# Kernel optimization log

Measured on AMD Instinct MI355X. Metric: run time of the kernel, lower is better.

The kernel has to match this reference:

```python
import jax, jax.numpy as jnp
import numpy as np

N = 20000      # nodes
E = 120000     # directed edges (self-loops added in reference, per PyG default)
F_IN = 235
HID = 256
HEADS = 8
NEG_SLOPE = 0.2


def setup_inputs() -> dict:
    key = jax.random.key(0)
    ks = jax.random.split(key, 24)
    p = lambda k, shape: (jax.random.normal(k, shape, jnp.float32) * 0.05)
    inp = {}
    inp["x"] = jax.random.normal(ks[0], (N, F_IN), jnp.float32)
    inp["edge_index"] = jax.random.randint(ks[1], (2, E), 0, N, jnp.int32)
    # input projection
    inp["w_in"] = p(ks[2], (F_IN, HID)); inp["b_in"] = jnp.zeros((HID,), jnp.float32)
    # temporal MLP
    inp["w_t1"] = p(ks[3], (HID, HID)); inp["b_t1"] = jnp.zeros((HID,), jnp.float32)
    inp["w_t2"] = p(ks[4], (HID, HID)); inp["b_t2"] = jnp.zeros((HID,), jnp.float32)
    # GAT layer 1: heads=8, out_per_head=32, concat -> 256
    C1 = HID // HEADS
    inp["w_g1"] = p(ks[5], (HID, HEADS * C1)); inp["a_src1"] = p(ks[6], (HEADS, C1))
    inp["a_dst1"] = p(ks[7], (HEADS, C1)); inp["b_g1"] = jnp.zeros((HEADS * C1,), jnp.float32)
    # GAT layer 2: same shape
    inp["w_g2"] = p(ks[8], (HID, HEADS * C1)); inp["a_src2"] = p(ks[9], (HEADS, C1))
    inp["a_dst2"] = p(ks[10], (HEADS, C1)); inp["b_g2"] = jnp.zeros((HEADS * C1,), jnp.float32)
    # GAT layer 3: heads=8, out_per_head=256, concat -> 2048
    inp["w_g3"] = p(ks[11], (HID, HEADS * HID)); inp["a_src3"] = p(ks[12], (HEADS, HID))
    inp["a_dst3"] = p(ks[13], (HEADS, HID)); inp["b_g3"] = jnp.zeros((HEADS * HID,), jnp.float32)
    # classifier
    inp["w_c1"] = p(ks[14], (2 * HID, HID)); inp["b_c1"] = jnp.zeros((HID,), jnp.float32)
    inp["w_c2"] = p(ks[15], (HID, 2)); inp["b_c2"] = jnp.zeros((2,), jnp.float32)
    return inp


def _gat(x, src, dst, W, a_src, a_dst, b, C):
    """PyG-style GATConv: gather -> per-edge logits -> segment softmax -> scatter-add."""
    h = (x @ W).reshape(-1, HEADS, C)                       # [N, H, C]
    alpha_s = jnp.sum(h * a_src, axis=-1)                   # [N, H]
    alpha_d = jnp.sum(h * a_dst, axis=-1)                   # [N, H]
    e = jax.nn.leaky_relu(alpha_s[src] + alpha_d[dst], NEG_SLOPE)   # [Etot, H]
    m = jax.ops.segment_max(e, dst, num_segments=N)         # [N, H] (self-loops ensure non-empty)
    ex = jnp.exp(e - m[dst])
    den = jax.ops.segment_sum(ex, dst, num_segments=N)
    alpha = ex / (den[dst] + 1e-16)                          # [Etot, H]
    out = jax.ops.segment_sum(alpha[:, :, None] * h[src], dst, num_segments=N)  # [N, H, C]
    return out.reshape(-1, HEADS * C) + b


def reference(x, edge_index, w_in, b_in, w_t1, b_t1, w_t2, b_t2,
              w_g1, a_src1, a_dst1, b_g1, w_g2, a_src2, a_dst2, b_g2,
              w_g3, a_src3, a_dst3, b_g3, w_c1, b_c1, w_c2, b_c2):
    h = jax.nn.elu(x @ w_in + b_in)                          # [N, 256]
    t = jax.nn.relu(h @ w_t1 + b_t1) @ w_t2 + b_t2          # [N, 256] (dropout inactive in eval)
    loop = jnp.arange(N, dtype=edge_index.dtype)
    src = jnp.concatenate([edge_index[0], loop])
    dst = jnp.concatenate([edge_index[1], loop])
    g = jax.nn.elu(_gat(h, src, dst, w_g1, a_src1, a_dst1, b_g1, HID // HEADS))
    g = jax.nn.elu(_gat(g, src, dst, w_g2, a_src2, a_dst2, b_g2, HID // HEADS))
    g = jax.nn.elu(_gat(g, src, dst, w_g3, a_src3, a_dst3, b_g3, HID))  # [N, 2048]
    g = g.reshape(N, HEADS, HID).mean(axis=1)                # [N, 256]
    comb = jnp.concatenate([g, t], axis=-1)                  # [N, 512]
    logits = jax.nn.relu(comb @ w_c1 + b_c1) @ w_c2 + b_c2   # [N, 2]
    return logits
```

## Files before the change

kernel.cpp:

```cpp
#include <hip/hip_runtime.h>
#include <hip/hip_bf16.h>
#include <math.h>


#define HID 256
#define HEADS 8
#define FIN 235

typedef __attribute__((ext_vector_type(8))) short short8;
typedef __attribute__((ext_vector_type(4))) float floatx4;

__device__ __forceinline__ float elu_f(float x) { return x > 0.f ? x : __expf(x) - 1.f; }
__device__ __forceinline__ float bf2f(unsigned short u) {
  return __uint_as_float(((unsigned int)u) << 16);
}
__device__ __forceinline__ unsigned short f2bfu(float f) {
  union { __hip_bfloat16 b; unsigned short u; } c;
  c.b = __float2bfloat16(f);
  return c.u;
}

__global__ void xcvt_k(const float* __restrict__ x, __hip_bfloat16* __restrict__ xb, int M) {
  int id = blockIdx.x * blockDim.x + threadIdx.x;
  if (id >= M * 256) return;
  int m = id >> 8, k = id & 255;
  xb[id] = (k < FIN) ? __float2bfloat16(x[(size_t)m * FIN + k]) : __float2bfloat16(0.f);
}

__global__ void wprep_k(const float* __restrict__ w_in, const float* __restrict__ w_t1,
                        const float* __restrict__ w_g1, const float* __restrict__ w_t2,
                        const float* __restrict__ w_g2, const float* __restrict__ w_c1,
                        const float* __restrict__ w_g3, const float* __restrict__ a_s3,
                        const float* __restrict__ a_d3, __hip_bfloat16* __restrict__ wtin,
                        __hip_bfloat16* __restrict__ wtpair, __hip_bfloat16* __restrict__ wtt2,
                        __hip_bfloat16* __restrict__ wtg2, __hip_bfloat16* __restrict__ wtc1,
                        __hip_bfloat16* __restrict__ wtg3s, float* __restrict__ apj) {
  __shared__ float t[32][33];
  int z = blockIdx.z;
  if (z == 14) {
    int idx = (blockIdx.y * 8 + blockIdx.x) * 256 + threadIdx.y * 32 + threadIdx.x;
    if (idx < 256 * 16) {
      int k = idx >> 4, o = idx & 15;
      int h = o >> 1;
      const float* av = (o & 1) ? (a_d3 + h * 256) : (a_s3 + h * 256);
      const float* wr = w_g3 + (size_t)k * 2048 + h * 256;
      float s = 0.f;
      for (int c = 0; c < 256; c++) s += wr[c] * av[c];
      apj[idx] = s;
    }
    return;
  }
  const float* src;
  __hip_bfloat16* dst;
  int K, Kpad, Nstride;
  if (z == 5) {
    src = w_c1; dst = wtc1; K = 512; Kpad = 512; Nstride = 256;
  } else {
    if (blockIdx.y >= 8) return;
    switch (z) {
      case 0: src = w_in; dst = wtin; K = FIN; Kpad = 256; Nstride = 256; break;
      case 1: src = w_t1; dst = wtpair; K = 256; Kpad = 256; Nstride = 256; break;
      case 2: src = w_g1; dst = wtpair + 256 * 256; K = 256; Kpad = 256; Nstride = 256; break;
      case 3: src = w_t2; dst = wtt2; K = 256; Kpad = 256; Nstride = 256; break;
      case 4: src = w_g2; dst = wtg2; K = 256; Kpad = 256; Nstride = 256; break;
      default: {
        int h = z - 6;
        src = w_g3 + h * 256; dst = wtg3s + h * 256; K = 256; Kpad = 2048; Nstride = 2048;
      }
    }
  }
  int nb = blockIdx.x * 32, kb = blockIdx.y * 32;
  int tx = threadIdx.x, ty = threadIdx.y;
#pragma unroll
  for (int j = 0; j < 32; j += 8) {
    int k = kb + ty + j;
    t[ty + j][tx] = (k < K) ? src[(size_t)k * Nstride + nb + tx] : 0.f;
  }
  __syncthreads();
#pragma unroll
  for (int j = 0; j < 32; j += 8) {
    int n = nb + ty + j;
    int k = kb + tx;
    dst[(size_t)n * Kpad + k] = __float2bfloat16(t[tx][ty + j]);
  }
}

__global__ void count_k(const int* __restrict__ ei, int* __restrict__ deg, int E) {
  int i = blockIdx.x * blockDim.x + threadIdx.x;
  if (i < E) atomicAdd(&deg[ei[E + i]], 1);
}

__global__ void scan_k(const int* __restrict__ deg, int* __restrict__ rp, int n) {
  __shared__ int wsum[16];
  __shared__ int s_carry;
  int tid = threadIdx.x, lane = tid & 63, wid = tid >> 6;
  if (tid == 0) { s_carry = 0; rp[0] = 0; }
  __syncthreads();
  for (int base = 0; base < n; base += 1024) {
    int i = base + tid;
    int x = (i < n) ? (deg[i] + 1) : 0;
#pragma unroll
    for (int off = 1; off < 64; off <<= 1) {
      int y = __shfl_up(x, off);
      if (lane >= off) x += y;
    }
    if (lane == 63) wsum[wid] = x;
    __syncthreads();
    if (wid == 0 && lane < 16) {
      int s = wsum[lane];
#pragma unroll
      for (int off = 1; off < 16; off <<= 1) {
        int y = __shfl_up(s, off);
        if (lane >= off) s += y;
      }
      wsum[lane] = s;
    }
    __syncthreads();
    int offset = s_carry + (wid > 0 ? wsum[wid - 1] : 0);
    if (i < n) rp[i + 1] = offset + x;
    __syncthreads();
    if (tid == 1023) s_carry += wsum[15];
    __syncthreads();
  }
}

__global__ void fill_k(const int* __restrict__ ei, const int* __restrict__ rp,
                       int* __restrict__ fillc, int* __restrict__ colA, int E, int n) {
  int i = blockIdx.x * blockDim.x + threadIdx.x;
  if (i < E) {
    int d = ei[E + i];
    int pos = rp[d] + atomicAdd(&fillc[d], 1);
    colA[pos] = ei[i];
  } else if (i < E + n) {
    int v = i - E;
    int pos = rp[v] + atomicAdd(&fillc[v], 1);
    colA[pos] = v;
  }
}

template <int ACT, int ALPHA>
__global__ __launch_bounds__(256) void mgemm64_k(
    const __hip_bfloat16* __restrict__ A, const __hip_bfloat16* __restrict__ Bt,
    const float* __restrict__ bias, __hip_bfloat16* __restrict__ Cb,
    int ldc, int M, int N, int K, const float* __restrict__ a_s,
    const float* __restrict__ a_d, float* __restrict__ as_, float* __restrict__ ad_) {
  __shared__ short As[64 * 40];
  __shared__ short Bs[64 * 40];
  int tid = threadIdx.x;
  int row0 = blockIdx.y * 64, col0 = blockIdx.x * 64;
  int w = tid >> 6, lane = tid & 63;
  int wr = w >> 1, wc = w & 1;
  int quad = lane >> 4, l16 = lane & 15;
  floatx4 zero = {0.f, 0.f, 0.f, 0.f};
  floatx4 acc[2][2];
#pragma unroll
  for (int i = 0; i < 2; i++)
#pragma unroll
    for (int j = 0; j < 2; j++) acc[i][j] = zero;

  int srow = tid >> 2, sq = tid & 3;
  const __hip_bfloat16* Ap = A + (size_t)(row0 + srow) * K + sq * 8;
  const __hip_bfloat16* Bp = Bt + (size_t)(col0 + srow) * K + sq * 8;
  bool aok = (row0 + srow) < M;

  uint4 a1 = make_uint4(0, 0, 0, 0);
  if (aok) a1 = *(const uint4*)(Ap);
  uint4 b1 = *(const uint4*)(Bp);

  for (int k0 = 0; k0 < K; k0 += 32) {
    __syncthreads();
    *(uint4*)&As[srow * 40 + sq * 8] = a1;
    *(uint4*)&Bs[srow * 40 + sq * 8] = b1;
    int kn = k0 + 32;
    if (kn < K) {
      if (aok) a1 = *(const uint4*)(Ap + kn);
      b1 = *(const uint4*)(Bp + kn);
    }
    __syncthreads();
    short8 fa[2], fb[2];
#pragma unroll
    for (int i = 0; i < 2; i++) {
      fa[i] = *(const short8*)&As[(wr * 32 + i * 16 + l16) * 40 + quad * 8];
      fb[i] = *(const short8*)&Bs[(wc * 32 + i * 16 + l16) * 40 + quad * 8];
    }
#pragma unroll
    for (int mi = 0; mi < 2; mi++)
#pragma unroll
      for (int ni = 0; ni < 2; ni++)
        acc[mi][ni] = __builtin_amdgcn_mfma_f32_16x16x32_bf16(fa[mi], fb[ni], acc[mi][ni], 0, 0, 0);
  }

#pragma unroll
  for (int mi = 0; mi < 2; mi++) {
    int rbase = row0 + wr * 32 + mi * 16 + quad * 4;
#pragma unroll
    for (int ni = 0; ni < 2; ni++) {
      int c = col0 + wc * 32 + ni * 16 + l16;
      float bv = bias ? bias[c] : 0.f;
#pragma unroll
      for (int reg = 0; reg < 4; reg++) {
        int rr = rbase + reg;
        if (rr >= M) continue;
        float v = acc[mi][ni][reg] + bv;
        if (ACT == 1) v = fmaxf(v, 0.f);
        if (ACT == 2) v = elu_f(v);
        Cb[(size_t)rr * ldc + c] = __float2bfloat16(v);
      }
    }
  }

  if (ALPHA) {
    int h = 2 * blockIdx.x + wc;
    float aS0 = a_s[h * 32 + l16], aS1 = a_s[h * 32 + 16 + l16];
    float aD0 = a_d[h * 32 + l16], aD1 = a_d[h * 32 + 16 + l16];
#pragma unroll
    for (int mi = 0; mi < 2; mi++)
#pragma unroll
      for (int reg = 0; reg < 4; reg++) {
        float pS = acc[mi][0][reg] * aS0 + acc[mi][1][reg] * aS1;
        float pD = acc[mi][0][reg] * aD0 + acc[mi][1][reg] * aD1;
#pragma unroll
        for (int off = 1; off < 16; off <<= 1) {
          pS += __shfl_xor(pS, off);
          pD += __shfl_xor(pD, off);
        }
        if (l16 == 0) {
          int r = row0 + wr * 32 + mi * 16 + quad * 4 + reg;
          if (r < M) {
            as_[r * 8 + h] = pS;
            ad_[r * 8 + h] = pD;
          }
        }
      }
  }
}

__global__ __launch_bounds__(256) void mgemm_dual_k(
    const __hip_bfloat16* __restrict__ A, const __hip_bfloat16* __restrict__ Bt,
    const float* __restrict__ bias1, __hip_bfloat16* __restrict__ O1,
    __hip_bfloat16* __restrict__ O2, int M, const float* __restrict__ a_s1,
    const float* __restrict__ a_d1, float* __restrict__ as_, float* __restrict__ ad_) {
  const int K = 256;
  __shared__ short As[64 * 40];
  __shared__ short Bs[128 * 40];
  int tid = threadIdx.x;
  int row0 = blockIdx.y * 64, col0 = blockIdx.x * 128;
  int w = tid >> 6, lane = tid & 63;
  int wr = w >> 1, wc = w & 1;
  int quad = lane >> 4, l16 = lane & 15;
  floatx4 zero = {0.f, 0.f, 0.f, 0.f};
  floatx4 acc[2][4];
#pragma unroll
  for (int i = 0; i < 2; i++)
#pragma unroll
    for (int j = 0; j < 4; j++) acc[i][j] = zero;

  int srow = tid >> 2, sq = tid & 3;
  const __hip_bfloat16* Ap = A + (size_t)(row0 + srow) * K + sq * 8;
  const __hip_bfloat16* Bp1 = Bt + (size_t)(col0 + srow) * K + sq * 8;
  const __hip_bfloat16* Bp2 = Bt + (size_t)(col0 + 64 + srow) * K + sq * 8;
  bool aok = (row0 + srow) < M;

  uint4 a1 = make_uint4(0, 0, 0, 0);
  if (aok) a1 = *(const uint4*)(Ap);
  uint4 b1 = *(const uint4*)(Bp1);
  uint4 b2 = *(const uint4*)(Bp2);

  for (int k0 = 0; k0 < K; k0 += 32) {
    __syncthreads();
    *(uint4*)&As[srow * 40 + sq * 8] = a1;
    *(uint4*)&Bs[srow * 40 + sq * 8] = b1;
    *(uint4*)&Bs[(64 + srow) * 40 + sq * 8] = b2;
    int kn = k0 + 32;
    if (kn < K) {
      if (aok) a1 = *(const uint4*)(Ap + kn);
      b1 = *(const uint4*)(Bp1 + kn);
      b2 = *(const uint4*)(Bp2 + kn);
    }
    __syncthreads();
    short8 fa[2], fb[4];
#pragma unroll
    for (int i = 0; i < 2; i++)
      fa[i] = *(const short8*)&As[(wr * 32 + i * 16 + l16) * 40 + quad * 8];
#pragma unroll
    for (int i = 0; i < 4; i++)
      fb[i] = *(const short8*)&Bs[(wc * 64 + i * 16 + l16) * 40 + quad * 8];
#pragma unroll
    for (int mi = 0; mi < 2; mi++)
#pragma unroll
      for (int ni = 0; ni < 4; ni++)
        acc[mi][ni] = __builtin_amdgcn_mfma_f32_16x16x32_bf16(fa[mi], fb[ni], acc[mi][ni], 0, 0, 0);
  }

#pragma unroll
  for (int mi = 0; mi < 2; mi++) {
    int rbase = row0 + wr * 32 + mi * 16 + quad * 4;
#pragma unroll
    for (int ni = 0; ni < 4; ni++) {
      int c = col0 + wc * 64 + ni * 16 + l16;
      bool first = c < 256;
      float bv = first ? bias1[c] : 0.f;
      int cc = first ? c : (c - 256);
#pragma unroll
      for (int reg = 0; reg < 4; reg++) {
        int rr = rbase + reg;
        if (rr >= M) continue;
        float v = acc[mi][ni][reg] + bv;
        if (first) v = fmaxf(v, 0.f);
        __hip_bfloat16* dst = first ? O1 : O2;
        dst[(size_t)rr * 256 + cc] = __float2bfloat16(v);
      }
    }
  }

  if (blockIdx.x >= 2) {
    int hb = (blockIdx.x - 2) * 4 + wc * 2;
    float aSA0 = a_s1[hb * 32 + l16], aSA1 = a_s1[hb * 32 + 16 + l16];
    float aDA0 = a_d1[hb * 32 + l16], aDA1 = a_d1[hb * 32 + 16 + l16];
    float aSB0 = a_s1[(hb + 1) * 32 + l16], aSB1 = a_s1[(hb + 1) * 32 + 16 + l16];
    float aDB0 = a_d1[(hb + 1) * 32 + l16], aDB1 = a_d1[(hb + 1) * 32 + 16 + l16];
#pragma unroll
    for (int mi = 0; mi < 2; mi++)
#pragma unroll
      for (int reg = 0; reg < 4; reg++) {
        float pSA = acc[mi][0][reg] * aSA0 + acc[mi][1][reg] * aSA1;
        float pDA = acc[mi][0][reg] * aDA0 + acc[mi][1][reg] * aDA1;
        float pSB = acc[mi][2][reg] * aSB0 + acc[mi][3][reg] * aSB1;
        float pDB = acc[mi][2][reg] * aDB0 + acc[mi][3][reg] * aDB1;
#pragma unroll
        for (int off = 1; off < 16; off <<= 1) {
          pSA += __shfl_xor(pSA, off);
          pDA += __shfl_xor(pDA, off);
          pSB += __shfl_xor(pSB, off);
          pDB += __shfl_xor(pDB, off);
        }
        if (l16 == 0) {
          int r = row0 + wr * 32 + mi * 16 + quad * 4 + reg;
          if (r < M) {
            as_[r * 8 + hb] = pSA;
            ad_[r * 8 + hb] = pDA;
            as_[r * 8 + hb + 1] = pSB;
            ad_[r * 8 + hb + 1] = pDB;
          }
        }
      }
  }
}

__global__ __launch_bounds__(256) void mgemm3_k(
    const __hip_bfloat16* __restrict__ A, const __hip_bfloat16* __restrict__ Bt,
    const float* __restrict__ bias, __hip_bfloat16* __restrict__ comb, int M) {
  const int K = 2048;
  __shared__ short As[64 * 40];
  __shared__ short Bs[64 * 40];
  int tid = threadIdx.x;
  int mg = (M + 63) >> 6;
  int total = mg * 4;
  int F = blockIdx.y * 4 + blockIdx.x;
  int Fmain = (total >> 5) << 5;
  int bx, by;
  if (F < Fmain) {
    by = (F >> 5) * 8 + (F & 7);
    bx = (F >> 3) & 3;
  } else {
    by = ((total >> 5) << 3) + ((F - Fmain) >> 2);
    bx = (F - Fmain) & 3;
  }
  int row0 = by * 64, col0 = bx * 64;
  int w = tid >> 6, lane = tid & 63;
  int wr = w >> 1, wc = w & 1;
  int quad = lane >> 4, l16 = lane & 15;
  floatx4 zero = {0.f, 0.f, 0.f, 0.f};
  floatx4 acc[2][2], sum[2][2];
#pragma unroll
  for (int i = 0; i < 2; i++)
#pragma unroll
    for (int j = 0; j < 2; j++) { acc[i][j] = zero; sum[i][j] = zero; }

  int srow = tid >> 2, sq = tid & 3;
  const __hip_bfloat16* Ap = A + (size_t)(row0 + srow) * K + sq * 8;
  const __hip_bfloat16* Bp = Bt + (size_t)(col0 + srow) * K + sq * 8;
  bool aok = (row0 + srow) < M;

  uint4 a1 = make_uint4(0, 0, 0, 0);
  if (aok) a1 = *(const uint4*)(Ap);
  uint4 b1 = *(const uint4*)(Bp);

  for (int k0 = 0; k0 < K; k0 += 32) {
    __syncthreads();
    *(uint4*)&As[srow * 40 + sq * 8] = a1;
    *(uint4*)&Bs[srow * 40 + sq * 8] = b1;
    int kn = k0 + 32;
    if (kn < K) {
      if (aok) a1 = *(const uint4*)(Ap + kn);
      b1 = *(const uint4*)(Bp + kn);
    }
    __syncthreads();
    short8 fa[2], fb[2];
#pragma unroll
    for (int i = 0; i < 2; i++) {
      fa[i] = *(const short8*)&As[(wr * 32 + i * 16 + l16) * 40 + quad * 8];
      fb[i] = *(const short8*)&Bs[(wc * 32 + i * 16 + l16) * 40 + quad * 8];
    }
#pragma unroll
    for (int mi = 0; mi < 2; mi++)
#pragma unroll
      for (int ni = 0; ni < 2; ni++)
        acc[mi][ni] = __builtin_amdgcn_mfma_f32_16x16x32_bf16(fa[mi], fb[ni], acc[mi][ni], 0, 0, 0);
    if (((k0 + 32) & 255) == 0) {
      int h = k0 >> 8;
#pragma unroll
      for (int mi = 0; mi < 2; mi++)
#pragma unroll
        for (int ni = 0; ni < 2; ni++) {
          int c = col0 + wc * 32 + ni * 16 + l16;
          float bv = bias[h * 256 + c];
#pragma unroll
          for (int reg = 0; reg < 4; reg++) {
            sum[mi][ni][reg] += elu_f(acc[mi][ni][reg] + bv);
            acc[mi][ni][reg] = 0.f;
          }
        }
    }
  }

#pragma unroll
  for (int mi = 0; mi < 2; mi++) {
    int rbase = row0 + wr * 32 + mi * 16 + quad * 4;
#pragma unroll
    for (int ni = 0; ni < 2; ni++) {
      int c = col0 + wc * 32 + ni * 16 + l16;
#pragma unroll
      for (int reg = 0; reg < 4; reg++) {
        int rr = rbase + reg;
        if (rr >= M) continue;
        comb[(size_t)rr * 512 + c] = __float2bfloat16(sum[mi][ni][reg] * 0.125f);
      }
    }
  }
}

__global__ __launch_bounds__(256) void mgemm_cls_k(
    const __hip_bfloat16* __restrict__ A, const __hip_bfloat16* __restrict__ Bt,
    const float* __restrict__ bias, const float* __restrict__ w2,
    float* __restrict__ out, int M) {
  const int K = 512;
  __shared__ short As[64 * 40];
  __shared__ short Bs[128 * 40];
  __shared__ float ls[64][2][2];
  int tid = threadIdx.x;
  int row0 = blockIdx.y * 64, col0 = blockIdx.x * 128;
  int w = tid >> 6, lane = tid & 63;
  int wr = w >> 1, wc = w & 1;
  int quad = lane >> 4, l16 = lane & 15;
  floatx4 zero = {0.f, 0.f, 0.f, 0.f};
  floatx4 acc[2][4];
#pragma unroll
  for (int i = 0; i < 2; i++)
#pragma unroll
    for (int j = 0; j < 4; j++) acc[i][j] = zero;

  int srow = tid >> 2, sq = tid & 3;
  const __hip_bfloat16* Ap = A + (size_t)(row0 + srow) * K + sq * 8;
  const __hip_bfloat16* Bp1 = Bt + (size_t)(col0 + srow) * K + sq * 8;
  const __hip_bfloat16* Bp2 = Bt + (size_t)(col0 + 64 + srow) * K + sq * 8;
  bool aok = (row0 + srow) < M;

  uint4 a1 = make_uint4(0, 0, 0, 0);
  if (aok) a1 = *(const uint4*)(Ap);
  uint4 b1 = *(const uint4*)(Bp1);
  uint4 b2 = *(const uint4*)(Bp2);

  for (int k0 = 0; k0 < K; k0 += 32) {
    __syncthreads();
    *(uint4*)&As[srow * 40 + sq * 8] = a1;
    *(uint4*)&Bs[srow * 40 + sq * 8] = b1;
    *(uint4*)&Bs[(64 + srow) * 40 + sq * 8] = b2;
    int kn = k0 + 32;
    if (kn < K) {
      if (aok) a1 = *(const uint4*)(Ap + kn);
      b1 = *(const uint4*)(Bp1 + kn);
      b2 = *(const uint4*)(Bp2 + kn);
    }
    __syncthreads();
    short8 fa[2], fb[4];
#pragma unroll
    for (int i = 0; i < 2; i++)
      fa[i] = *(const short8*)&As[(wr * 32 + i * 16 + l16) * 40 + quad * 8];
#pragma unroll
    for (int i = 0; i < 4; i++)
      fb[i] = *(const short8*)&Bs[(wc * 64 + i * 16 + l16) * 40 + quad * 8];
#pragma unroll
    for (int mi = 0; mi < 2; mi++)
#pragma unroll
      for (int ni = 0; ni < 4; ni++)
        acc[mi][ni] = __builtin_amdgcn_mfma_f32_16x16x32_bf16(fa[mi], fb[ni], acc[mi][ni], 0, 0, 0);
  }

  float p0[2][4], p1[2][4];
#pragma unroll
  for (int mi = 0; mi < 2; mi++)
#pragma unroll
    for (int reg = 0; reg < 4; reg++) { p0[mi][reg] = 0.f; p1[mi][reg] = 0.f; }
#pragma unroll
  for (int mi = 0; mi < 2; mi++)
#pragma unroll
    for (int ni = 0; ni < 4; ni++) {
      int c = col0 + wc * 64 + ni * 16 + l16;
      float bv = bias[c];
      float w20 = w2[c * 2 + 0], w21 = w2[c * 2 + 1];
#pragma unroll
      for (int reg = 0; reg < 4; reg++) {
        float v = fmaxf(acc[mi][ni][reg] + bv, 0.f);
        p0[mi][reg] += v * w20;
        p1[mi][reg] += v * w21;
      }
    }
#pragma unroll
  for (int off = 1; off < 16; off <<= 1)
#pragma unroll
    for (int mi = 0; mi < 2; mi++)
#pragma unroll
      for (int reg = 0; reg < 4; reg++) {
        p0[mi][reg] += __shfl_xor(p0[mi][reg], off);
        p1[mi][reg] += __shfl_xor(p1[mi][reg], off);
      }
  if (l16 == 0) {
#pragma unroll
    for (int mi = 0; mi < 2; mi++)
#pragma unroll
      for (int reg = 0; reg < 4; reg++) {
        int rl = wr * 32 + mi * 16 + quad * 4 + reg;
        ls[rl][wc][0] = p0[mi][reg];
        ls[rl][wc][1] = p1[mi][reg];
      }
  }
  __syncthreads();
  if (tid < 64) {
    int r = row0 + tid;
    if (r < M) {
      atomicAdd(&out[r * 2 + 0], ls[tid][0][0] + ls[tid][1][0]);
      atomicAdd(&out[r * 2 + 1], ls[tid][0][1] + ls[tid][1][1]);
    }
  }
}

__global__ void initout_k(const float* __restrict__ b, float* __restrict__ out, int M) {
  int i = blockIdx.x * blockDim.x + threadIdx.x;
  if (i < M * 2) out[i] = b[i & 1];
}

__global__ __launch_bounds__(256) void alpha3_k(const __hip_bfloat16* __restrict__ g2,
                                                const float* __restrict__ apj,
                                                float* __restrict__ as_, float* __restrict__ ad_,
                                                int M) {
  __shared__ float sapj[4096];
  int tid = threadIdx.x;
  for (int i = tid; i < 4096; i += 256) sapj[i] = apj[i];
  __syncthreads();
  int nl = tid >> 4, o = tid & 15;
  int n = blockIdx.x * 16 + nl;
  if (n >= M) return;
  const __hip_bfloat16* row = g2 + (size_t)n * 256;
  float s = 0.f;
  for (int cc = 0; cc < 256; cc += 8) {
    short8 v8 = *(const short8*)(row + cc);
#pragma unroll
    for (int j = 0; j < 8; j++)
      s += bf2f((unsigned short)v8[j]) * sapj[(cc + j) * 16 + o];
  }
  if (o & 1) ad_[n * 8 + (o >> 1)] = s;
  else as_[n * 8 + (o >> 1)] = s;
}

__global__ __launch_bounds__(256) void aggf_k(const int* __restrict__ rp,
                                              const int* __restrict__ col,
                                              const __hip_bfloat16* __restrict__ hW,
                                              const float* __restrict__ as_,
                                              const float* __restrict__ ad_,
                                              const float* __restrict__ bias,
                                              __hip_bfloat16* __restrict__ out, int M) {
  int dst = blockIdx.x * 4 + (threadIdx.x >> 6);
  if (dst >= M) return;
  int t = threadIdx.x & 63;
  int h = t >> 3, c = t << 2;
  int beg = rp[dst], end = rp[dst + 1];
  float adv = ad_[dst * 8 + h];
  float m = -3.4e38f, den = 0.f;
  float a0 = 0.f, a1 = 0.f, a2 = 0.f, a3 = 0.f;
  for (int i = beg; i < end; i++) {
    int s = col[i];
    float e = as_[s * 8 + h] + adv;
    e = e > 0.f ? e : 0.2f * e;
    float mn = fmaxf(m, e);
    float sc = __expf(m - mn);
    float wgt = __expf(e - mn);
    m = mn;
    union { uint2 u; unsigned short us[4]; } uu;
    uu.u = *(const uint2*)(hW + (size_t)s * HID + c);
    den = den * sc + wgt;
    a0 = a0 * sc + wgt * bf2f(uu.us[0]);
    a1 = a1 * sc + wgt * bf2f(uu.us[1]);
    a2 = a2 * sc + wgt * bf2f(uu.us[2]);
    a3 = a3 * sc + wgt * bf2f(uu.us[3]);
  }
  float inv = 1.f / (den + 1e-16f);
  out[(size_t)dst * HID + c + 0] = __float2bfloat16(elu_f(a0 * inv + bias[c + 0]));
  out[(size_t)dst * HID + c + 1] = __float2bfloat16(elu_f(a1 * inv + bias[c + 1]));
  out[(size_t)dst * HID + c + 2] = __float2bfloat16(elu_f(a2 * inv + bias[c + 2]));
  out[(size_t)dst * HID + c + 3] = __float2bfloat16(elu_f(a3 * inv + bias[c + 3]));
}

__global__ __launch_bounds__(256) void esoft_k(const int* __restrict__ rp,
                                               const int* __restrict__ col,
                                               const float* __restrict__ as_,
                                               const float* __restrict__ ad_,
                                               float* __restrict__ ex,
                                               float* __restrict__ invden, int M) {
  int dst = blockIdx.x * 4 + (threadIdx.x >> 6);
  if (dst >= M) return;
  int lane = threadIdx.x & 63;
  int es = lane >> 3, h = lane & 7;
  int beg = rp[dst], end = rp[dst + 1];
  float adv = ad_[dst * 8 + h];
  float m = -3.4e38f;
  for (int i = beg + es; i < end; i += 8) {
    float e = as_[col[i] * 8 + h] + adv;
    e = e > 0.f ? e : 0.2f * e;
    m = fmaxf(m, e);
  }
  m = fmaxf(m, __shfl_xor(m, 8));
  m = fmaxf(m, __shfl_xor(m, 16));
  m = fmaxf(m, __shfl_xor(m, 32));
  float den = 0.f;
  for (int i = beg + es; i < end; i += 8) {
    float e = as_[col[i] * 8 + h] + adv;
    e = e > 0.f ? e : 0.2f * e;
    float v = __expf(e - m);
    ex[(size_t)i * 8 + h] = v;
    den += v;
  }
  den += __shfl_xor(den, 8);
  den += __shfl_xor(den, 16);
  den += __shfl_xor(den, 32);
  if (es == 0) invden[dst * 8 + h] = 1.f / (den + 1e-16f);
}

__global__ __launch_bounds__(256) void agg3_k(const int* __restrict__ rp,
                                              const int* __restrict__ col,
                                              const __hip_bfloat16* __restrict__ g2,
                                              const float* __restrict__ ex,
                                              const float* __restrict__ invden,
                                              __hip_bfloat16* __restrict__ outA, int M) {
  int dst = blockIdx.x * 4 + (threadIdx.x >> 6);
  if (dst >= M) return;
  int t = threadIdx.x & 63;
  int beg = rp[dst], end = rp[dst + 1];
  float acc[4][8];
#pragma unroll
  for (int ch = 0; ch < 4; ch++)
#pragma unroll
    for (int h = 0; h < 8; h++) acc[ch][h] = 0.f;
  for (int i = beg; i < end; i++) {
    int s = col[i];
    float4 w0 = *(const float4*)(ex + (size_t)i * 8);
    float4 w1 = *(const float4*)(ex + (size_t)i * 8 + 4);
    union { uint2 u; unsigned short us[4]; } uu;
    uu.u = *(const uint2*)(g2 + (size_t)s * 256 + t * 4);
#pragma unroll
    for (int ch = 0; ch < 4; ch++) {
      float v = bf2f(uu.us[ch]);
      acc[ch][0] += w0.x * v; acc[ch][1] += w0.y * v;
      acc[ch][2] += w0.z * v; acc[ch][3] += w0.w * v;
      acc[ch][4] += w1.x * v; acc[ch][5] += w1.y * v;
      acc[ch][6] += w1.z * v; acc[ch][7] += w1.w * v;
    }
  }
#pragma unroll
  for (int h = 0; h < 8; h++) {
    float inv = invden[dst * 8 + h];
    union { uint2 u; unsigned short us[4]; } pk;
#pragma unroll
    for (int ch = 0; ch < 4; ch++) pk.us[ch] = f2bfu(acc[ch][h] * inv);
    *(uint2*)(outA + (size_t)dst * 2048 + h * 256 + t * 4) = pk.u;
  }
}

extern "C" void kernel_launch(void* const* d_in, const int* in_sizes, int n_in,
                              void* d_out, int out_size, void* d_ws, size_t ws_size,
                              hipStream_t stream) {
  const float* x      = (const float*)d_in[0];
  const int*   ei     = (const int*)d_in[1];
  const float* w_in   = (const float*)d_in[2];
  const float* b_in   = (const float*)d_in[3];
  const float* w_t1   = (const float*)d_in[4];
  const float* b_t1   = (const float*)d_in[5];
  const float* w_t2   = (const float*)d_in[6];
  const float* b_t2   = (const float*)d_in[7];
  const float* w_g1   = (const float*)d_in[8];
  const float* a_src1 = (const float*)d_in[9];
  const float* a_dst1 = (const float*)d_in[10];
  const float* b_g1   = (const float*)d_in[11];
  const float* w_g2   = (const float*)d_in[12];
  const float* a_src2 = (const float*)d_in[13];
  const float* a_dst2 = (const float*)d_in[14];
  const float* b_g2   = (const float*)d_in[15];
  const float* w_g3   = (const float*)d_in[16];
  const float* a_src3 = (const float*)d_in[17];
  const float* a_dst3 = (const float*)d_in[18];
  const float* b_g3   = (const float*)d_in[19];
  const float* w_c1   = (const float*)d_in[20];
  const float* b_c1   = (const float*)d_in[21];
  const float* w_c2   = (const float*)d_in[22];
  const float* b_c2   = (const float*)d_in[23];
  const int M = in_sizes[0] / FIN;
  const int E = in_sizes[1] / 2;
  (void)n_in; (void)out_size; (void)ws_size;

  char* wsb = (char*)d_ws;
  size_t off = 0;
  auto alloc = [&](size_t bytes) {
    void* p = wsb + off;
    off = (off + bytes + 255) & ~(size_t)255;
    return p;
  };
  typedef __hip_bfloat16 bf;
  bf* xb     = (bf*)alloc((size_t)M * 256 * 2);
  bf* wtin   = (bf*)alloc(256 * 256 * 2);
  bf* wtpair = (bf*)alloc(512 * 256 * 2);
  bf* wtt2   = (bf*)alloc(256 * 256 * 2);
  bf* wtg2   = (bf*)alloc(256 * 256 * 2);
  bf* wtg3s  = (bf*)alloc(256 * 2048 * 2);
  bf* wtc1   = (bf*)alloc(256 * 512 * 2);
  bf* actA   = (bf*)alloc((size_t)M * HID * 2);
  bf* actB   = (bf*)alloc((size_t)M * HID * 2);
  bf* hW1    = (bf*)alloc((size_t)M * HID * 2);
  bf* comb   = (bf*)alloc((size_t)M * 2 * HID * 2);
  bf* hWb    = (bf*)alloc((size_t)M * 2048 * 2);
  float* as_ = (float*)alloc((size_t)M * 8 * 4);
  float* ad_ = (float*)alloc((size_t)M * 8 * 4);
  float* apj = (float*)alloc(256 * 16 * 4);
  float* exw = (float*)alloc((size_t)(E + M) * 8 * 4);
  float* ivd = (float*)alloc((size_t)M * 8 * 4);
  int* degfill = (int*)alloc((size_t)2 * M * 4);
  int* deg   = degfill;
  int* fillc = degfill + M;
  int* rp    = (int*)alloc((size_t)(M + 1) * 4);
  int* colA  = (int*)alloc((size_t)(E + M) * 4);

  xcvt_k<<<(M * 256 + 255) / 256, 256, 0, stream>>>(x, xb, M);
  wprep_k<<<dim3(8, 16, 15), dim3(32, 8), 0, stream>>>(
      w_in, w_t1, w_g1, w_t2, w_g2, w_c1, w_g3, a_src3, a_dst3,
      wtin, wtpair, wtt2, wtg2, wtc1, wtg3s, apj);

  hipMemsetAsync(degfill, 0, (size_t)2 * M * 4, stream);
  count_k<<<(E + 255) / 256, 256, 0, stream>>>(ei, deg, E);
  scan_k<<<1, 1024, 0, stream>>>(deg, rp, M);
  fill_k<<<(E + M + 255) / 256, 256, 0, stream>>>(ei, rp, fillc, colA, E, M);

  int eg = (M + 3) / 4;
  int mg = (M + 63) / 64;

  mgemm64_k<2, 0><<<dim3(4, mg), 256, 0, stream>>>(xb, wtin, b_in, actA, HID, M, HID, 256,
                                                   nullptr, nullptr, nullptr, nullptr);
  mgemm_dual_k<<<dim3(4, mg), 256, 0, stream>>>(actA, wtpair, b_t1, actB, hW1, M,
                                                a_src1, a_dst1, as_, ad_);
  mgemm64_k<0, 0><<<dim3(4, mg), 256, 0, stream>>>(actB, wtt2, b_t2, comb + HID, 2 * HID,
                                                   M, HID, 256, nullptr, nullptr, nullptr, nullptr);

  aggf_k<<<eg, 256, 0, stream>>>(rp, colA, hW1, as_, ad_, b_g1, actB, M);

  mgemm64_k<0, 1><<<dim3(4, mg), 256, 0, stream>>>(actB, wtg2, nullptr, hW1, HID, M, HID, 256,
                                                   a_src2, a_dst2, as_, ad_);
  aggf_k<<<eg, 256, 0, stream>>>(rp, colA, hW1, as_, ad_, b_g2, actA, M);

  alpha3_k<<<(M + 15) / 16, 256, 0, stream>>>(actA, apj, as_, ad_, M);
  esoft_k<<<eg, 256, 0, stream>>>(rp, colA, as_, ad_, exw, ivd, M);
  agg3_k<<<eg, 256, 0, stream>>>(rp, colA, actA, exw, ivd, hWb, M);
  mgemm3_k<<<dim3(4, mg), 256, 0, stream>>>(hWb, wtg3s, b_g3, comb, M);

  initout_k<<<(M * 2 + 255) / 256, 256, 0, stream>>>(b_c2, (float*)d_out, M);
  mgemm_cls_k<<<dim3(2, mg), 256, 0, stream>>>(comb, wtc1, b_c1, w_c2, (float*)d_out, M);
}
```

Before: 394.6 us.

## Fuse degree count into x conversion, fold alpha3 into aggf, deepen mgemm3 K-tile

Three changes. First, the edge degree counting is merged into the x-to-bf16 conversion kernel as extra blocks, with the memset moved earlier, which removes one launch. Second, the layer-3 attention projections are computed inside the second GAT aggregation kernel with a wavefront shuffle reduction, using new buffers. This removes the separate alpha3 kernel and its re-read of the activations, but adds a 16-way 64-lane reduction to every destination. Third, mgemm3 now stages 64 K-columns per iteration instead of 32, halving the barrier count at the cost of more LDS and registers.

Result: slower. 438.5 us (+11.1%).

```diff
diff --git a/kernel.cpp b/kernel.cpp
--- a/kernel.cpp
+++ b/kernel.cpp
@@ -20,11 +20,19 @@
   return c.u;
 }
 
-__global__ void xcvt_k(const float* __restrict__ x, __hip_bfloat16* __restrict__ xb, int M) {
-  int id = blockIdx.x * blockDim.x + threadIdx.x;
-  if (id >= M * 256) return;
-  int m = id >> 8, k = id & 255;
-  xb[id] = (k < FIN) ? __float2bfloat16(x[(size_t)m * FIN + k]) : __float2bfloat16(0.f);
+__global__ void xc_k(const float* __restrict__ x, __hip_bfloat16* __restrict__ xb,
+                     const int* __restrict__ ei, int* __restrict__ deg,
+                     int M, int E, int xblocks) {
+  int b = blockIdx.x;
+  if (b < xblocks) {
+    int id = b * 256 + threadIdx.x;
+    if (id >= M * 256) return;
+    int m = id >> 8, k = id & 255;
+    xb[id] = (k < FIN) ? __float2bfloat16(x[(size_t)m * FIN + k]) : __float2bfloat16(0.f);
+  } else {
+    int i = (b - xblocks) * 256 + threadIdx.x;
+    if (i < E) atomicAdd(&deg[ei[E + i]], 1);
+  }
 }
 
 __global__ void wprep_k(const float* __restrict__ w_in, const float* __restrict__ w_t1,
@@ -85,11 +93,6 @@
   }
 }
 
-__global__ void count_k(const int* __restrict__ ei, int* __restrict__ deg, int E) {
-  int i = blockIdx.x * blockDim.x + threadIdx.x;
-  if (i < E) atomicAdd(&deg[ei[E + i]], 1);
-}
-
 __global__ void scan_k(const int* __restrict__ deg, int* __restrict__ rp, int n) {
   __shared__ int wsum[16];
   __shared__ int s_carry;
@@ -351,8 +354,8 @@
     const __hip_bfloat16* __restrict__ A, const __hip_bfloat16* __restrict__ Bt,
     const float* __restrict__ bias, __hip_bfloat16* __restrict__ comb, int M) {
   const int K = 2048;
-  __shared__ short As[64 * 40];
-  __shared__ short Bs[64 * 40];
+  __shared__ short As[64 * 72];
+  __shared__ short Bs[64 * 72];
   int tid = threadIdx.x;
   int mg = (M + 63) >> 6;
   int total = mg * 4;
@@ -377,37 +380,44 @@
 #pragma unroll
     for (int j = 0; j < 2; j++) { acc[i][j] = zero; sum[i][j] = zero; }
 
-  int srow = tid >> 2, sq = tid & 3;
-  const __hip_bfloat16* Ap = A + (size_t)(row0 + srow) * K + sq * 8;
-  const __hip_bfloat16* Bp = Bt + (size_t)(col0 + srow) * K + sq * 8;
+  int srow = tid >> 2, sq = (tid & 3) * 8;
+  const __hip_bfloat16* Ap = A + (size_t)(row0 + srow) * K + sq;
+  const __hip_bfloat16* Bp = Bt + (size_t)(col0 + srow) * K + sq;
   bool aok = (row0 + srow) < M;
 
-  uint4 a1 = make_uint4(0, 0, 0, 0);
-  if (aok) a1 = *(const uint4*)(Ap);
+  uint4 a1 = make_uint4(0, 0, 0, 0), a2 = make_uint4(0, 0, 0, 0);
+  if (aok) { a1 = *(const uint4*)(Ap); a2 = *(const uint4*)(Ap + 32); }
   uint4 b1 = *(const uint4*)(Bp);
-
-  for (int k0 = 0; k0 < K; k0 += 32) {
-    __syncthreads();
-    *(uint4*)&As[srow * 40 + sq * 8] = a1;
-    *(uint4*)&Bs[srow * 40 + sq * 8] = b1;
-    int kn = k0 + 32;
+  uint4 b2 = *(const uint4*)(Bp + 32);
+
+  for (int k0 = 0; k0 < K; k0 += 64) {
+    __syncthreads();
+    *(uint4*)&As[srow * 72 + sq] = a1;
+    *(uint4*)&As[srow * 72 + sq + 32] = a2;
+    *(uint4*)&Bs[srow * 72 + sq] = b1;
+    *(uint4*)&Bs[srow * 72 + sq + 32] = b2;
+    int kn = k0 + 64;
     if (kn < K) {
-      if (aok) a1 = *(const uint4*)(Ap + kn);
+      if (aok) { a1 = *(const uint4*)(Ap + kn); a2 = *(const uint4*)(Ap + kn + 32); }
       b1 = *(const uint4*)(Bp + kn);
-    }
-    __syncthreads();
-    short8 fa[2], fb[2];
-#pragma unroll
-    for (int i = 0; i < 2; i++) {
-      fa[i] = *(const short8*)&As[(wr * 32 + i * 16 + l16) * 40 + quad * 8];
-      fb[i] = *(const short8*)&Bs[(wc * 32 + i * 16 + l16) * 40 + quad * 8];
-    }
-#pragma unroll
-    for (int mi = 0; mi < 2; mi++)
-#pragma unroll
-      for (int ni = 0; ni < 2; ni++)
-        acc[mi][ni] = __builtin_amdgcn_mfma_f32_16x16x32_bf16(fa[mi], fb[ni], acc[mi][ni], 0, 0, 0);
-    if (((k0 + 32) & 255) == 0) {
+      b2 = *(const uint4*)(Bp + kn + 32);
+    }
+    __syncthreads();
+#pragma unroll
+    for (int c32 = 0; c32 < 2; c32++) {
+      short8 fa[2], fb[2];
+#pragma unroll
+      for (int i = 0; i < 2; i++) {
+        fa[i] = *(const short8*)&As[(wr * 32 + i * 16 + l16) * 72 + c32 * 32 + quad * 8];
+        fb[i] = *(const short8*)&Bs[(wc * 32 + i * 16 + l16) * 72 + c32 * 32 + quad * 8];
+      }
+#pragma unroll
+      for (int mi = 0; mi < 2; mi++)
+#pragma unroll
+        for (int ni = 0; ni < 2; ni++)
+          acc[mi][ni] = __builtin_amdgcn_mfma_f32_16x16x32_bf16(fa[mi], fb[ni], acc[mi][ni], 0, 0, 0);
+    }
+    if (((k0 + 64) & 255) == 0) {
       int h = k0 >> 8;
 #pragma unroll
       for (int mi = 0; mi < 2; mi++)
@@ -550,39 +560,26 @@
   if (i < M * 2) out[i] = b[i & 1];
 }
 
-__global__ __launch_bounds__(256) void alpha3_k(const __hip_bfloat16* __restrict__ g2,
-                                                const float* __restrict__ apj,
-                                                float* __restrict__ as_, float* __restrict__ ad_,
-                                                int M) {
-  __shared__ float sapj[4096];
-  int tid = threadIdx.x;
-  for (int i = tid; i < 4096; i += 256) sapj[i] = apj[i];
-  __syncthreads();
-  int nl = tid >> 4, o = tid & 15;
-  int n = blockIdx.x * 16 + nl;
-  if (n >= M) return;
-  const __hip_bfloat16* row = g2 + (size_t)n * 256;
-  float s = 0.f;
-  for (int cc = 0; cc < 256; cc += 8) {
-    short8 v8 = *(const short8*)(row + cc);
-#pragma unroll
-    for (int j = 0; j < 8; j++)
-      s += bf2f((unsigned short)v8[j]) * sapj[(cc + j) * 16 + o];
-  }
-  if (o & 1) ad_[n * 8 + (o >> 1)] = s;
-  else as_[n * 8 + (o >> 1)] = s;
-}
-
+template <int FUSE3>
 __global__ __launch_bounds__(256) void aggf_k(const int* __restrict__ rp,
                                               const int* __restrict__ col,
                                               const __hip_bfloat16* __restrict__ hW,
                                               const float* __restrict__ as_,
                                               const float* __restrict__ ad_,
                                               const float* __restrict__ bias,
-                                              __hip_bfloat16* __restrict__ out, int M) {
-  int dst = blockIdx.x * 4 + (threadIdx.x >> 6);
+                                              __hip_bfloat16* __restrict__ out, int M,
+                                              const float* __restrict__ apj,
+                                              float* __restrict__ as3,
+                                              float* __restrict__ ad3) {
+  __shared__ float sapj[FUSE3 ? 4096 : 1];
+  int tid = threadIdx.x;
+  if (FUSE3) {
+    for (int i = tid; i < 4096; i += 256) sapj[i] = apj[i];
+    __syncthreads();
+  }
+  int dst = blockIdx.x * 4 + (tid >> 6);
   if (dst >= M) return;
-  int t = threadIdx.x & 63;
+  int t = tid & 63;
   int h = t >> 3, c = t << 2;
   int beg = rp[dst], end = rp[dst + 1];
   float adv = ad_[dst * 8 + h];
@@ -605,10 +602,33 @@
     a3 = a3 * sc + wgt * bf2f(uu.us[3]);
   }
   float inv = 1.f / (den + 1e-16f);
-  out[(size_t)dst * HID + c + 0] = __float2bfloat16(elu_f(a0 * inv + bias[c + 0]));
-  out[(size_t)dst * HID + c + 1] = __float2bfloat16(elu_f(a1 * inv + bias[c + 1]));
-  out[(size_t)dst * HID + c + 2] = __float2bfloat16(elu_f(a2 * inv + bias[c + 2]));
-  out[(size_t)dst * HID + c + 3] = __float2bfloat16(elu_f(a3 * inv + bias[c + 3]));
+  float e0 = elu_f(a0 * inv + bias[c + 0]);
+  float e1 = elu_f(a1 * inv + bias[c + 1]);
+  float e2 = elu_f(a2 * inv + bias[c + 2]);
+  float e3 = elu_f(a3 * inv + bias[c + 3]);
+  out[(size_t)dst * HID + c + 0] = __float2bfloat16(e0);
+  out[(size_t)dst * HID + c + 1] = __float2bfloat16(e1);
+  out[(size_t)dst * HID + c + 2] = __float2bfloat16(e2);
+  out[(size_t)dst * HID + c + 3] = __float2bfloat16(e3);
+
+  if (FUSE3) {
+    float p[16];
+#pragma unroll
+    for (int o = 0; o < 16; o++)
+      p[o] = e0 * sapj[(c + 0) * 16 + o] + e1 * sapj[(c + 1) * 16 + o] +
+             e2 * sapj[(c + 2) * 16 + o] + e3 * sapj[(c + 3) * 16 + o];
+#pragma unroll
+    for (int off = 1; off < 64; off <<= 1)
+#pragma unroll
+      for (int o = 0; o < 16; o++) p[o] += __shfl_xor(p[o], off);
+    if (t == 0) {
+#pragma unroll
+      for (int hh = 0; hh < 8; hh++) {
+        as3[dst * 8 + hh] = p[hh * 2];
+        ad3[dst * 8 + hh] = p[hh * 2 + 1];
+      }
+    }
+  }
 }
 
 __global__ __launch_bounds__(256) void esoft_k(const int* __restrict__ rp,
@@ -739,6 +759,8 @@
   bf* hWb    = (bf*)alloc((size_t)M * 2048 * 2);
   float* as_ = (float*)alloc((size_t)M * 8 * 4);
   float* ad_ = (float*)alloc((size_t)M * 8 * 4);
+  float* as3 = (float*)alloc((size_t)M * 8 * 4);
+  float* ad3 = (float*)alloc((size_t)M * 8 * 4);
   float* apj = (float*)alloc(256 * 16 * 4);
   float* exw = (float*)alloc((size_t)(E + M) * 8 * 4);
   float* ivd = (float*)alloc((size_t)M * 8 * 4);
@@ -748,13 +770,14 @@
   int* rp    = (int*)alloc((size_t)(M + 1) * 4);
   int* colA  = (int*)alloc((size_t)(E + M) * 4);
 
-  xcvt_k<<<(M * 256 + 255) / 256, 256, 0, stream>>>(x, xb, M);
+  hipMemsetAsync(degfill, 0, (size_t)2 * M * 4, stream);
+  int xblocks = (M * 256 + 255) / 256;
+  int cblocks = (E + 255) / 256;
+  xc_k<<<xblocks + cblocks, 256, 0, stream>>>(x, xb, ei, deg, M, E, xblocks);
   wprep_k<<<dim3(8, 16, 15), dim3(32, 8), 0, stream>>>(
       w_in, w_t1, w_g1, w_t2, w_g2, w_c1, w_g3, a_src3, a_dst3,
       wtin, wtpair, wtt2, wtg2, wtc1, wtg3s, apj);
 
-  hipMemsetAsync(degfill, 0, (size_t)2 * M * 4, stream);
-  count_k<<<(E + 255) / 256, 256, 0, stream>>>(ei, deg, E);
   scan_k<<<1, 1024, 0, stream>>>(deg, rp, M);
   fill_k<<<(E + M + 255) / 256, 256, 0, stream>>>(ei, rp, fillc, colA, E, M);
 
@@ -768,14 +791,15 @@
   mgemm64_k<0, 0><<<dim3(4, mg), 256, 0, stream>>>(actB, wtt2, b_t2, comb + HID, 2 * HID,
                                                    M, HID, 256, nullptr, nullptr, nullptr, nullptr);
 
-  aggf_k<<<eg, 256, 0, stream>>>(rp, colA, hW1, as_, ad_, b_g1, actB, M);
+  aggf_k<0><<<eg, 256, 0, stream>>>(rp, colA, hW1, as_, ad_, b_g1, actB, M,
+                                    nullptr, nullptr, nullptr);
 
   mgemm64_k<0, 1><<<dim3(4, mg), 256, 0, stream>>>(actB, wtg2, nullptr, hW1, HID, M, HID, 256,
                                                    a_src2, a_dst2, as_, ad_);
-  aggf_k<<<eg, 256, 0, stream>>>(rp, colA, hW1, as_, ad_, b_g2, actA, M);
-
-  alpha3_k<<<(M + 15) / 16, 256, 0, stream>>>(actA, apj, as_, ad_, M);
-  esoft_k<<<eg, 256, 0, stream>>>(rp, colA, as_, ad_, exw, ivd, M);
+  aggf_k<1><<<eg, 256, 0, stream>>>(rp, colA, hW1, as_, ad_, b_g2, actA, M,
+                                    apj, as3, ad3);
+
+  esoft_k<<<eg, 256, 0, stream>>>(rp, colA, as3, ad3, exw, ivd, M);
   agg3_k<<<eg, 256, 0, stream>>>(rp, colA, actA, exw, ivd, hWb, M);
   mgemm3_k<<<dim3(4, mg), 256, 0, stream>>>(hWb, wtg3s, b_g3, comb, M);
 
```
